# Optimization experiments

Measured on AMD Instinct MI355X. Metric: run time of the kernel, lower is better.

## Reference

```python
import jax, jax.numpy as jnp
import numpy as np

B, MAX_NODES, NODE_D, STATE_D, D_MODEL = 16384, 20, 128, 128, 128


def _ragged_layout():
    # Deterministic ragged node counts in [5, 20], avg 12.5 -> total 204800.
    counts = 5 + (np.arange(B) % 16)            # [B]
    total = int(counts.sum())                    # 204800
    off = np.concatenate([[0], np.cumsum(counts)[:-1]])  # exclusive offsets
    slots = np.arange(MAX_NODES)[None, :]        # [1, M]
    valid = slots < counts[:, None]              # [B, M] bool
    gidx = off[:, None] + np.minimum(slots, counts[:, None] - 1)  # [B, M]
    # Reverse map: global node i (graph b, slot s) -> flat index b*M + s
    within = np.arange(total) - np.repeat(off, counts)
    rev = np.repeat(np.arange(B), counts) * MAX_NODES + within     # [total]
    return gidx.astype(np.int32), valid.astype(np.float32), rev.astype(np.int32), total


def setup_inputs() -> dict:
    key = jax.random.key(0)
    k1, k2, k3, k4 = jax.random.split(key, 4)
    gidx, valid, rev, total = _ragged_layout()
    scale_q = 1.0 / np.sqrt(STATE_D)
    scale_k = 1.0 / np.sqrt(NODE_D)
    return {
        "state_embed": jax.random.normal(k1, (B, STATE_D), dtype=jnp.float32),
        "action_embed": jax.random.normal(k2, (total, NODE_D), dtype=jnp.float32),
        "wq": jax.random.normal(k3, (STATE_D, D_MODEL), dtype=jnp.float32) * scale_q,
        "wk": jax.random.normal(k4, (NODE_D, D_MODEL), dtype=jnp.float32) * scale_k,
        "gather_idx": jnp.asarray(gidx),
        "valid_mask": jnp.asarray(valid),
        "rev_idx": jnp.asarray(rev),
    }


def reference(state_embed, action_embed, wq, wk, gather_idx, valid_mask, rev_idx):
    # q_on_all=True path, training=False (dropout = identity).
    # pad_node_param sparse matmul == masked gather into [B, MAX_NODES, NODE_D]
    padded = action_embed[gather_idx] * valid_mask[..., None]   # [B, M, NODE_D]
    q = state_embed @ wq                                         # [B, d_model]
    k = padded @ wk                                              # [B, M, d_model]
    scores = jnp.einsum("bd,bmd->bm", q, k)                      # [B, M]
    flat = scores.reshape(-1)                                    # [B*M]
    # pad_reverse_param sparse matmul == gather back to ragged node list
    return flat[rev_idx][:, None]                                # [total_nodes, 1]
```

## Files before the change

### kernel.cpp

```cpp
#include <hip/hip_runtime.h>


__global__ __launch_bounds__(256) void k1_weights(const float* __restrict__ wq,
                                                  const float* __restrict__ wk,
                                                  float* __restrict__ M) {
    int idx = blockIdx.x * 256 + threadIdx.x;
    int d = idx >> 7, e = idx & 127;
    const float4* q4 = reinterpret_cast<const float4*>(wq + (size_t)d * 128);
    const float4* w4 = reinterpret_cast<const float4*>(wk + (size_t)e * 128);
    float acc = 0.f;
#pragma unroll
    for (int k = 0; k < 32; ++k) {
        float4 a = q4[k], b = w4[k];
        acc += a.x * b.x + a.y * b.y + a.z * b.z + a.w * b.w;
    }
    M[idx] = acc;
}

constexpr int GPB  = 32;
constexpr int NPB  = 400;
constexpr int SSTR = 132;

__global__ __launch_bounds__(256) void k_fused(const float* __restrict__ state,
                                               const float* __restrict__ M,
                                               const float* __restrict__ action,
                                               const int* __restrict__ rev,
                                               float* __restrict__ out) {
    __shared__ float sS[GPB * SSTR];
    __shared__ float sT[GPB * SSTR];
    const int tid = threadIdx.x;
    const int b0 = blockIdx.x * GPB;

#pragma unroll
    for (int rep = 0; rep < 4; ++rep) {
        int f = (rep * 256 + tid) * 4;
        int g = f >> 7, d = f & 127;
        float4 v = *reinterpret_cast<const float4*>(state + (size_t)(b0 + g) * 128 + d);
        *reinterpret_cast<float4*>(sS + g * SSTR + d) = v;
    }
    __syncthreads();

    {
        const int w  = tid >> 6;
        const int e0 = (tid & 63) * 2;
        float a0[8], a1[8];
#pragma unroll
        for (int i = 0; i < 8; ++i) { a0[i] = 0.f; a1[i] = 0.f; }
        for (int d4 = 0; d4 < 128; d4 += 4) {
            float4 s[8];
#pragma unroll
            for (int i = 0; i < 8; ++i)
                s[i] = *reinterpret_cast<const float4*>(sS + (w * 8 + i) * SSTR + d4);
#pragma unroll
            for (int dd = 0; dd < 4; ++dd) {
                float2 m = *reinterpret_cast<const float2*>(M + (size_t)(d4 + dd) * 128 + e0);
#pragma unroll
                for (int i = 0; i < 8; ++i) {
                    float sv = (dd == 0) ? s[i].x : (dd == 1) ? s[i].y : (dd == 2) ? s[i].z : s[i].w;
                    a0[i] += sv * m.x;
                    a1[i] += sv * m.y;
                }
            }
        }
#pragma unroll
        for (int i = 0; i < 8; ++i)
            *reinterpret_cast<float2*>(sT + (w * 8 + i) * SSTR + e0) = make_float2(a0[i], a1[i]);
    }
    __syncthreads();

    const int node0 = blockIdx.x * NPB;
    for (int idx = tid; idx < NPB * 8; idx += 256) {
        int nl = idx >> 3, ln = idx & 7;
        int node = node0 + nl;
        int g = rev[node] / 20 - b0;
        const float* arow = action + (size_t)node * 128;
        const float* trow = sT + g * SSTR;
        float acc = 0.f;
#pragma unroll
        for (int i = 0; i < 4; ++i) {
            int d = ln * 4 + i * 32;
            float4 a = *reinterpret_cast<const float4*>(arow + d);
            float4 x = *reinterpret_cast<const float4*>(trow + d);
            acc += a.x * x.x + a.y * x.y + a.z * x.z + a.w * x.w;
        }
        acc += __shfl_xor(acc, 1);
        acc += __shfl_xor(acc, 2);
        acc += __shfl_xor(acc, 4);
        if (ln == 0) out[node] = acc;
    }
}

extern "C" void kernel_launch(void* const* d_in, const int* in_sizes, int n_in,
                              void* d_out, int out_size, void* d_ws, size_t ws_size,
                              hipStream_t stream) {
    const float* state  = (const float*)d_in[0];
    const float* action = (const float*)d_in[1];
    const float* wq     = (const float*)d_in[2];
    const float* wk     = (const float*)d_in[3];
    const int*   rev    = (const int*)d_in[6];
    float* out = (float*)d_out;

    const int B = in_sizes[0] / 128;
    float* M = (float*)d_ws;

    k1_weights<<<(128 * 128) / 256, 256, 0, stream>>>(wq, wk, M);
    k_fused<<<B / GPB, 256, 0, stream>>>(state, M, action, rev, out);
}
```

Measured before the change: 35.15 us.

## Split fused kernel into separate projection and scoring kernels via global workspace

The fused per-block kernel that computed state projections into shared memory and then scored nodes is split into two kernels. One computes t = state·M for all graphs into a global workspace, and a second, fully parallel kernel scores each node with one 8-thread group per node. This removes the heavy per-block serial node loop and allows many more blocks for latency hiding. In exchange it adds a kernel launch and a global round trip for t (about 8 MB written and read back).

```diff
diff --git a/kernel.cpp b/kernel.cpp
--- a/kernel.cpp
+++ b/kernel.cpp
@@ -17,77 +17,75 @@
     M[idx] = acc;
 }
 
-constexpr int GPB  = 32;
-constexpr int NPB  = 400;
+constexpr int RPB  = 32;
 constexpr int SSTR = 132;
 
-__global__ __launch_bounds__(256) void k_fused(const float* __restrict__ state,
-                                               const float* __restrict__ M,
-                                               const float* __restrict__ action,
-                                               const int* __restrict__ rev,
-                                               float* __restrict__ out) {
-    __shared__ float sS[GPB * SSTR];
-    __shared__ float sT[GPB * SSTR];
+__global__ __launch_bounds__(256) void k2_t(const float* __restrict__ state,
+                                            const float* __restrict__ M,
+                                            float* __restrict__ t) {
+    __shared__ float sS[RPB * SSTR];
     const int tid = threadIdx.x;
-    const int b0 = blockIdx.x * GPB;
+    const int r0b = blockIdx.x * RPB;
 
 #pragma unroll
     for (int rep = 0; rep < 4; ++rep) {
         int f = (rep * 256 + tid) * 4;
         int g = f >> 7, d = f & 127;
-        float4 v = *reinterpret_cast<const float4*>(state + (size_t)(b0 + g) * 128 + d);
+        float4 v = *reinterpret_cast<const float4*>(state + (size_t)(r0b + g) * 128 + d);
         *reinterpret_cast<float4*>(sS + g * SSTR + d) = v;
     }
     __syncthreads();
 
-    {
-        const int w  = tid >> 6;
-        const int e0 = (tid & 63) * 2;
-        float a0[8], a1[8];
+    const int w  = tid >> 6;
+    const int e0 = (tid & 63) * 2;
+    float a0[8], a1[8];
 #pragma unroll
-        for (int i = 0; i < 8; ++i) { a0[i] = 0.f; a1[i] = 0.f; }
-        for (int d4 = 0; d4 < 128; d4 += 4) {
-            float4 s[8];
+    for (int i = 0; i < 8; ++i) { a0[i] = 0.f; a1[i] = 0.f; }
+    for (int d4 = 0; d4 < 128; d4 += 4) {
+        float4 s[8];
 #pragma unroll
-            for (int i = 0; i < 8; ++i)
-                s[i] = *reinterpret_cast<const float4*>(sS + (w * 8 + i) * SSTR + d4);
+        for (int i = 0; i < 8; ++i)
+            s[i] = *reinterpret_cast<const float4*>(sS + (w * 8 + i) * SSTR + d4);
 #pragma unroll
-            for (int dd = 0; dd < 4; ++dd) {
-                float2 m = *reinterpret_cast<const float2*>(M + (size_t)(d4 + dd) * 128 + e0);
+        for (int dd = 0; dd < 4; ++dd) {
+            float2 m = *reinterpret_cast<const float2*>(M + (size_t)(d4 + dd) * 128 + e0);
 #pragma unroll
-                for (int i = 0; i < 8; ++i) {
-                    float sv = (dd == 0) ? s[i].x : (dd == 1) ? s[i].y : (dd == 2) ? s[i].z : s[i].w;
-                    a0[i] += sv * m.x;
-                    a1[i] += sv * m.y;
-                }
+            for (int i = 0; i < 8; ++i) {
+                float sv = (dd == 0) ? s[i].x : (dd == 1) ? s[i].y : (dd == 2) ? s[i].z : s[i].w;
+                a0[i] += sv * m.x;
+                a1[i] += sv * m.y;
             }
         }
+    }
 #pragma unroll
-        for (int i = 0; i < 8; ++i)
-            *reinterpret_cast<float2*>(sT + (w * 8 + i) * SSTR + e0) = make_float2(a0[i], a1[i]);
+    for (int i = 0; i < 8; ++i)
+        *reinterpret_cast<float2*>(t + (size_t)(r0b + w * 8 + i) * 128 + e0) =
+            make_float2(a0[i], a1[i]);
+}
+
+__global__ __launch_bounds__(256) void k3_scores(const float* __restrict__ action,
+                                                 const float* __restrict__ t,
+                                                 const int* __restrict__ rev,
+                                                 float* __restrict__ out,
+                                                 int n_nodes) {
+    int g = blockIdx.x * 256 + threadIdx.x;
+    int node = g >> 3, ln = g & 7;
+    if (node >= n_nodes) return;
+    int b = rev[node] / 20;
+    const float* arow = action + (size_t)node * 128;
+    const float* trow = t + (size_t)b * 128;
+    float acc = 0.f;
+#pragma unroll
+    for (int i = 0; i < 4; ++i) {
+        int d = ln * 4 + i * 32;
+        float4 a = *reinterpret_cast<const float4*>(arow + d);
+        float4 x = *reinterpret_cast<const float4*>(trow + d);
+        acc += a.x * x.x + a.y * x.y + a.z * x.z + a.w * x.w;
     }
-    __syncthreads();
-
-    const int node0 = blockIdx.x * NPB;
-    for (int idx = tid; idx < NPB * 8; idx += 256) {
-        int nl = idx >> 3, ln = idx & 7;
-        int node = node0 + nl;
-        int g = rev[node] / 20 - b0;
-        const float* arow = action + (size_t)node * 128;
-        const float* trow = sT + g * SSTR;
-        float acc = 0.f;
-#pragma unroll
-        for (int i = 0; i < 4; ++i) {
-            int d = ln * 4 + i * 32;
-            float4 a = *reinterpret_cast<const float4*>(arow + d);
-            float4 x = *reinterpret_cast<const float4*>(trow + d);
-            acc += a.x * x.x + a.y * x.y + a.z * x.z + a.w * x.w;
-        }
-        acc += __shfl_xor(acc, 1);
-        acc += __shfl_xor(acc, 2);
-        acc += __shfl_xor(acc, 4);
-        if (ln == 0) out[node] = acc;
-    }
+    acc += __shfl_xor(acc, 1);
+    acc += __shfl_xor(acc, 2);
+    acc += __shfl_xor(acc, 4);
+    if (ln == 0) out[node] = acc;
 }
 
 extern "C" void kernel_launch(void* const* d_in, const int* in_sizes, int n_in,
@@ -101,8 +99,12 @@
     float* out = (float*)d_out;
 
     const int B = in_sizes[0] / 128;
+    const int n_nodes = in_sizes[6];
+
     float* M = (float*)d_ws;
+    float* t = (float*)((char*)d_ws + 65536);
 
     k1_weights<<<(128 * 128) / 256, 256, 0, stream>>>(wq, wk, M);
-    k_fused<<<B / GPB, 256, 0, stream>>>(state, M, action, rev, out);
+    k2_t<<<B / RPB, 256, 0, stream>>>(state, M, t);
+    k3_scores<<<(n_nodes * 8 + 255) / 256, 256, 0, stream>>>(action, t, rev, out, n_nodes);
 }
```

After: 44.33 us. 26.1% more time.

## Double block size to 512 threads and unroll node dot-products two per thread

Applied to the files above, without the earlier changes.

Raises the fused kernel's block to 512 threads, remapping the state-times-M stage so each thread computes one output column for 8 graphs instead of two columns. The node scoring loop now processes two nodes per iteration, issuing all action and sT loads up front to increase memory-level parallelism. This is meant to hide global load latency on the action stream and raise occupancy. It adds register pressure, and the launch_bounds(512,4) hint may force spills.

```diff
diff --git a/kernel.cpp b/kernel.cpp
--- a/kernel.cpp
+++ b/kernel.cpp
@@ -21,72 +21,90 @@
 constexpr int NPB  = 400;
 constexpr int SSTR = 132;
 
-__global__ __launch_bounds__(256) void k_fused(const float* __restrict__ state,
-                                               const float* __restrict__ M,
-                                               const float* __restrict__ action,
-                                               const int* __restrict__ rev,
-                                               float* __restrict__ out) {
+__global__ __launch_bounds__(512, 4) void k_fused(const float* __restrict__ state,
+                                                  const float* __restrict__ M,
+                                                  const float* __restrict__ action,
+                                                  const int* __restrict__ rev,
+                                                  float* __restrict__ out) {
     __shared__ float sS[GPB * SSTR];
     __shared__ float sT[GPB * SSTR];
     const int tid = threadIdx.x;
-    const int b0 = blockIdx.x * GPB;
+    const int b0  = blockIdx.x * GPB;
 
-#pragma unroll
-    for (int rep = 0; rep < 4; ++rep) {
-        int f = (rep * 256 + tid) * 4;
+    {
+        int f = tid * 8;
         int g = f >> 7, d = f & 127;
-        float4 v = *reinterpret_cast<const float4*>(state + (size_t)(b0 + g) * 128 + d);
-        *reinterpret_cast<float4*>(sS + g * SSTR + d) = v;
+        float4 v0 = *reinterpret_cast<const float4*>(state + (size_t)(b0 + g) * 128 + d);
+        float4 v1 = *reinterpret_cast<const float4*>(state + (size_t)(b0 + g) * 128 + d + 4);
+        *reinterpret_cast<float4*>(sS + g * SSTR + d)     = v0;
+        *reinterpret_cast<float4*>(sS + g * SSTR + d + 4) = v1;
     }
     __syncthreads();
 
     {
-        const int w  = tid >> 6;
-        const int e0 = (tid & 63) * 2;
-        float a0[8], a1[8];
+        const int w    = tid >> 6;
+        const int p    = w >> 1;
+        const int half = w & 1;
+        const int e    = half * 64 + (tid & 63);
+        const int g0   = p * 8;
+        float acc[8];
 #pragma unroll
-        for (int i = 0; i < 8; ++i) { a0[i] = 0.f; a1[i] = 0.f; }
+        for (int i = 0; i < 8; ++i) acc[i] = 0.f;
         for (int d4 = 0; d4 < 128; d4 += 4) {
             float4 s[8];
 #pragma unroll
             for (int i = 0; i < 8; ++i)
-                s[i] = *reinterpret_cast<const float4*>(sS + (w * 8 + i) * SSTR + d4);
+                s[i] = *reinterpret_cast<const float4*>(sS + (g0 + i) * SSTR + d4);
 #pragma unroll
             for (int dd = 0; dd < 4; ++dd) {
-                float2 m = *reinterpret_cast<const float2*>(M + (size_t)(d4 + dd) * 128 + e0);
+                float m = M[(size_t)(d4 + dd) * 128 + e];
 #pragma unroll
                 for (int i = 0; i < 8; ++i) {
                     float sv = (dd == 0) ? s[i].x : (dd == 1) ? s[i].y : (dd == 2) ? s[i].z : s[i].w;
-                    a0[i] += sv * m.x;
-                    a1[i] += sv * m.y;
+                    acc[i] += sv * m;
                 }
             }
         }
 #pragma unroll
-        for (int i = 0; i < 8; ++i)
-            *reinterpret_cast<float2*>(sT + (w * 8 + i) * SSTR + e0) = make_float2(a0[i], a1[i]);
+        for (int i = 0; i < 8; ++i) sT[(g0 + i) * SSTR + e] = acc[i];
     }
     __syncthreads();
 
     const int node0 = blockIdx.x * NPB;
-    for (int idx = tid; idx < NPB * 8; idx += 256) {
-        int nl = idx >> 3, ln = idx & 7;
-        int node = node0 + nl;
-        int g = rev[node] / 20 - b0;
-        const float* arow = action + (size_t)node * 128;
-        const float* trow = sT + g * SSTR;
-        float acc = 0.f;
+    for (int base = tid; base < NPB * 8; base += 1024) {
+        int t0 = base, t1 = base + 512;
+        bool has1 = t1 < NPB * 8;
+        int n0 = t0 >> 3, l0 = t0 & 7;
+        int n1 = has1 ? (t1 >> 3) : n0;
+        int l1 = t1 & 7;
+        int g0n = rev[node0 + n0] / 20 - b0;
+        int g1n = rev[node0 + n1] / 20 - b0;
+        const float* ar0 = action + (size_t)(node0 + n0) * 128;
+        const float* ar1 = action + (size_t)(node0 + n1) * 128;
+
+        float4 a0[4], a1[4];
 #pragma unroll
-        for (int i = 0; i < 4; ++i) {
-            int d = ln * 4 + i * 32;
-            float4 a = *reinterpret_cast<const float4*>(arow + d);
-            float4 x = *reinterpret_cast<const float4*>(trow + d);
-            acc += a.x * x.x + a.y * x.y + a.z * x.z + a.w * x.w;
-        }
-        acc += __shfl_xor(acc, 1);
-        acc += __shfl_xor(acc, 2);
-        acc += __shfl_xor(acc, 4);
-        if (ln == 0) out[node] = acc;
+        for (int i = 0; i < 4; ++i) a0[i] = *reinterpret_cast<const float4*>(ar0 + l0 * 4 + i * 32);
+#pragma unroll
+        for (int i = 0; i < 4; ++i) a1[i] = *reinterpret_cast<const float4*>(ar1 + l1 * 4 + i * 32);
+        float4 x0[4], x1[4];
+#pragma unroll
+        for (int i = 0; i < 4; ++i) x0[i] = *reinterpret_cast<const float4*>(sT + g0n * SSTR + l0 * 4 + i * 32);
+#pragma unroll
+        for (int i = 0; i < 4; ++i) x1[i] = *reinterpret_cast<const float4*>(sT + g1n * SSTR + l1 * 4 + i * 32);
+
+        float acc0 = 0.f, acc1 = 0.f;
+#pragma unroll
+        for (int i = 0; i < 4; ++i)
+            acc0 += a0[i].x * x0[i].x + a0[i].y * x0[i].y + a0[i].z * x0[i].z + a0[i].w * x0[i].w;
+#pragma unroll
+        for (int i = 0; i < 4; ++i)
+            acc1 += a1[i].x * x1[i].x + a1[i].y * x1[i].y + a1[i].z * x1[i].z + a1[i].w * x1[i].w;
+
+        acc0 += __shfl_xor(acc0, 1); acc0 += __shfl_xor(acc0, 2); acc0 += __shfl_xor(acc0, 4);
+        acc1 += __shfl_xor(acc1, 1); acc1 += __shfl_xor(acc1, 2); acc1 += __shfl_xor(acc1, 4);
+        if (l0 == 0) out[node0 + n0] = acc0;
+        if (has1 && l1 == 0) out[node0 + n1] = acc1;
     }
 }
 
@@ -104,5 +122,5 @@
     float* M = (float*)d_ws;
 
     k1_weights<<<(128 * 128) / 256, 256, 0, stream>>>(wq, wk, M);
-    k_fused<<<B / GPB, 256, 0, stream>>>(state, M, action, rev, out);
+    k_fused<<<B / GPB, 512, 0, stream>>>(state, M, action, rev, out);
 }
```

New measurement: 35.63 us. No clear change (+1.4%).
